# Kernel tuning notes

Measured on AMD Instinct MI355X. Metric: run time of the kernel, lower is better.

The kernel has to match this reference:

```python
import jax, jax.numpy as jnp
import numpy as np

DIM = 512
HEADS = 8
B, H, W = 8, 32, 32
SMOOTH = 1e-4
BN_EPS = 1e-5


def _conv(x, w, pad):
    return jax.lax.conv_general_dilated(
        x, w, window_strides=(1, 1), padding=[(pad, pad), (pad, pad)],
        dimension_numbers=('NCHW', 'OIHW', 'NCHW'))


def setup_inputs() -> dict:
    key = jax.random.key(0)
    k1, k2, k3 = jax.random.split(key, 3)
    x = jax.random.normal(k1, (B, DIM, H, W), dtype=jnp.float32)
    # conv weights with fan-in style scaling for stable magnitudes
    W_qkv = jax.random.normal(k2, (3 * DIM, DIM, 3, 3), dtype=jnp.float32) * (1.0 / np.sqrt(DIM * 9))
    W_out = jax.random.normal(k3, (DIM, DIM, 1, 1), dtype=jnp.float32) * (1.0 / np.sqrt(DIM))
    gamma = jnp.ones((DIM,), dtype=jnp.float32)
    beta = jnp.zeros((DIM,), dtype=jnp.float32)
    return {"x": x, "W_qkv": W_qkv, "W_out": W_out, "gamma": gamma, "beta": beta}


def reference(x, W_qkv, W_out, gamma, beta):
    b, c, h, w = x.shape
    g = HEADS
    d = c // g
    n = h * w
    qkv = _conv(x, W_qkv, pad=1)                      # [b, 3c, h, w]
    q, k, v = jnp.split(qkv, 3, axis=1)
    # 'b (g d) h w -> b g (h w) d'
    to_seq = lambda t: t.reshape(b, g, d, n).transpose(0, 1, 3, 2)
    q, k, v = to_seq(q), to_seq(k), to_seq(v)         # [b, g, n, d]
    attn = jnp.einsum('bgid,bgjd->bgij', q, k)        # [b, g, n, n]
    qn = jnp.sqrt(jnp.sum(q * q, axis=-1) + SMOOTH)   # [b, g, n]
    kn = jnp.sqrt(jnp.sum(k * k, axis=-1) + SMOOTH)   # [b, g, n]
    attn = attn / (qn[:, :, :, None] * kn[:, :, None, :] + SMOOTH)
    out = jnp.einsum('bgij,bgjd->bgid', attn, v)      # [b, g, n, d]
    # 'b g (h w) d -> b (g d) h w'
    out = out.transpose(0, 1, 3, 2).reshape(b, c, h, w)
    out = _conv(out, W_out, pad=0)
    # BatchNorm2d (training mode: batch statistics, biased variance)
    mean = jnp.mean(out, axis=(0, 2, 3))
    var = jnp.var(out, axis=(0, 2, 3))
    out = (out - mean[None, :, None, None]) * jax.lax.rsqrt(var + BN_EPS)[None, :, None, None]
    out = out * gamma[None, :, None, None] + beta[None, :, None, None]
    return jax.nn.relu(out)
```

## Files before the change

kernel.cpp:

```cpp
#include <hip/hip_runtime.h>
#include <math.h>


#define SMOOTH 1e-4f
#define BN_EPS 1e-5f

typedef __attribute__((ext_vector_type(8))) short bf16x8;
typedef __attribute__((ext_vector_type(8))) unsigned short u16x8;
typedef __attribute__((ext_vector_type(4))) float f32x4;
typedef __attribute__((ext_vector_type(4))) unsigned int u32x4;
typedef __attribute__((ext_vector_type(4))) unsigned short u16x4;

__device__ inline unsigned short bf16rne(float f) {
  unsigned int u = __float_as_uint(f);
  u += 0x7fff + ((u >> 16) & 1);
  return (unsigned short)(u >> 16);
}
__device__ inline float b2f(unsigned short u) {
  return __uint_as_float((unsigned int)u << 16);
}

typedef __attribute__((address_space(1))) void gvoid;
typedef __attribute__((address_space(3))) void lvoid;
__device__ __forceinline__ void async16(const void* g, void* l) {
  __builtin_amdgcn_global_load_lds((gvoid*)g, (lvoid*)l, 16, 0, 0);
}

__global__ void prep_kernel(const float* __restrict__ wq,
                            unsigned short* __restrict__ wqr2,
                            const float* __restrict__ x,
                            unsigned short* __restrict__ xrp2,
                            const float* __restrict__ wo,
                            unsigned short* __restrict__ wor,
                            float* __restrict__ sums,
                            float* __restrict__ sumsq) {
  __shared__ float Sh[64 * 132];
  const int tid = threadIdx.x;
  const int bid = blockIdx.x;
  if (bid < 3072) {
    const size_t pair0 = (size_t)bid * 256;
    for (int off = tid; off < 576; off += 256)
      *(float4*)(Sh + off * 4) = *(const float4*)(wq + pair0 * 9 + off * 4);
    __syncthreads();
    const int co = (int)(pair0 >> 9);
    const int ciBase = (int)(pair0 & 511);
    const int cotile = co >> 6, co_l = co & 63;
    for (int idx = tid; idx < 288; idx += 256) {
      int t = idx >> 5;
      int oct = idx & 31;
      int ci = ciBase + oct * 8;
      int ci0c = ci >> 5, c4 = oct & 3;
      u16x8 pk;
#pragma unroll
      for (int e = 0; e < 8; ++e) pk[e] = bf16rne(Sh[(oct * 8 + e) * 9 + t]);
      size_t o = (size_t)(ci0c * 24 + cotile) * 18432 +
                 (size_t)((c4 * 9 + t) * 64 + co_l) * 8;
      *(u16x8*)(wqr2 + o) = pk;
    }
  } else if (bid < 3584) {
    const int bx = bid - 3072;
    const int p0 = (bx & 7) * 128;
    const int ci0 = ((bx >> 3) & 7) * 64;
    const int b = bx >> 6;
    for (int k = 0; k < 8; ++k) {
      int idx = tid + k * 256;
      int c4 = idx & 31, row = idx >> 5;
      *(float4*)(Sh + row * 132 + c4 * 4) =
          *(const float4*)(x + ((size_t)(b * 512 + ci0 + row)) * 1024 + p0 + c4 * 4);
    }
    __syncthreads();
    const int pl = tid >> 1, half = tid & 1;
    const int p = p0 + pl;
    const int h = p >> 5, w = p & 31;
#pragma unroll
    for (int v = 0; v < 8; ++v) {
      u16x4 pk;
#pragma unroll
      for (int e = 0; e < 4; ++e)
        pk[e] = bf16rne(Sh[(half * 32 + v * 4 + e) * 132 + pl]);
      int cc = ci0 + half * 32 + v * 4;
      int ci0c = cc >> 5, c4 = (cc >> 3) & 3, e0 = cc & 7;
      size_t gran =
          (size_t)((ci0c * 4 + c4) * 8 + b) * 1156 + (h + 1) * 34 + (w + 1);
      *(u16x4*)(xrp2 + gran * 8 + e0) = pk;
    }
  } else {
    const int rb = bid - 3584;
    int idx = rb * 256 + tid;
    wor[idx] = bf16rne(wo[idx]);
    if (rb < 2) {
      sums[idx] = 0.f;
      sumsq[idx] = 0.f;
    }
  }
}

__global__ __launch_bounds__(256) void conv3x3_mfma(
    const unsigned short* __restrict__ wqr2,
    const unsigned short* __restrict__ xrp2,
    unsigned short* __restrict__ qt, unsigned short* __restrict__ kt,
    unsigned short* __restrict__ vt, float* __restrict__ rqn,
    float* __restrict__ rkn) {
  __shared__ __align__(16) unsigned short Wl[2304 * 8];
  __shared__ __align__(16) unsigned short Xl[4 * 256 * 8];
  __shared__ float Snl[128];

  const int tid = threadIdx.x;
  const int lane = tid & 63;
  const int wave = tid >> 6;
  const int wco = (wave & 1) * 32;
  const int wn = (wave >> 1) * 64;
  const int l15 = lane & 15;
  const int quad = lane >> 4;
  const int h0 = blockIdx.x * 4;
  const int co0 = blockIdx.y * 64;
  const int b = blockIdx.z;

  f32x4 acc[2][4];
  for (int ma = 0; ma < 2; ++ma)
    for (int nb = 0; nb < 4; ++nb) acc[ma][nb] = (f32x4){0.f, 0.f, 0.f, 0.f};

  for (int ci0 = 0; ci0 < 512; ci0 += 32) {
    const int ci0c = ci0 >> 5;
    __syncthreads();
    const unsigned short* wsrc =
        wqr2 + (size_t)(ci0c * 24 + (co0 >> 6)) * 18432;
    {
      int cbase = wave * 9;
#pragma unroll
      for (int j = 0; j < 9; ++j) {
        int c = cbase + j;
        async16(wsrc + (size_t)c * 512 + lane * 8, Wl + (size_t)c * 512);
      }
    }
    const unsigned short* xsrc =
        xrp2 + ((size_t)((ci0c * 4 + wave) * 8 + b) * 1156 + h0 * 34) * 8;
#pragma unroll
    for (int j = 0; j < 4; ++j)
      async16(xsrc + (size_t)j * 512 + lane * 8,
              Xl + (size_t)(wave * 256 + j * 64) * 8);
    __syncthreads();

#pragma unroll
    for (int t = 0; t < 9; ++t) {
      const int ky = t / 3, kx = t - ky * 3;
      bf16x8 af[2], bfr[4];
#pragma unroll
      for (int ma = 0; ma < 2; ++ma)
        af[ma] = *(const bf16x8*)(
            Wl + (size_t)((quad * 9 + t) * 64 + wco + ma * 16 + l15) * 8);
#pragma unroll
      for (int nb = 0; nb < 4; ++nb) {
        int n = wn + nb * 16 + l15;
        int hh = (n >> 5) + ky;
        int wi = (n & 31) + kx;
        bfr[nb] = *(const bf16x8*)(Xl + (size_t)(quad * 256 + hh * 34 + wi) * 8);
      }
#pragma unroll
      for (int ma = 0; ma < 2; ++ma)
#pragma unroll
        for (int nb = 0; nb < 4; ++nb)
          acc[ma][nb] = __builtin_amdgcn_mfma_f32_16x16x32_bf16(
              af[ma], bfr[nb], acc[ma][nb], 0, 0, 0);
    }
  }

  const int sec = co0 >> 9;
  const int g = (co0 & 511) >> 6;
  const int bg = b * 8 + g;
  if (sec < 2) {
    unsigned short* dst = (sec == 0) ? qt : kt;
#pragma unroll
    for (int ma = 0; ma < 2; ++ma)
#pragma unroll
      for (int nb = 0; nb < 4; ++nb) {
        int n = wn + nb * 16 + l15;
        int p = (h0 + (n >> 5)) * 32 + (n & 31);
        int db = wco + ma * 16 + quad * 4;
        u16x4 pk;
#pragma unroll
        for (int r = 0; r < 4; ++r) pk[r] = bf16rne(acc[ma][nb][r]);
        *(u16x4*)(dst + ((size_t)bg * 1024 + p) * 64 + db) = pk;
      }
    float ps[4];
#pragma unroll
    for (int nb = 0; nb < 4; ++nb) {
      float s = 0.f;
#pragma unroll
      for (int ma = 0; ma < 2; ++ma)
#pragma unroll
        for (int r = 0; r < 4; ++r) s = fmaf(acc[ma][nb][r], acc[ma][nb][r], s);
      s += __shfl_down(s, 32);
      s += __shfl_down(s, 16);
      ps[nb] = s;
    }
    if (wco == 0 && quad == 0)
#pragma unroll
      for (int nb = 0; nb < 4; ++nb) Snl[wn + nb * 16 + l15] = ps[nb];
    __syncthreads();
    if (wco == 32 && quad == 0) {
      float* ndst = (sec == 0) ? rqn : rkn;
#pragma unroll
      for (int nb = 0; nb < 4; ++nb) {
        int n = wn + nb * 16 + l15;
        int p = (h0 + (n >> 5)) * 32 + (n & 31);
        ndst[bg * 1024 + p] = rsqrtf(Snl[n] + ps[nb] + SMOOTH);
      }
    }
  } else {
#pragma unroll
    for (int ma = 0; ma < 2; ++ma)
#pragma unroll
      for (int nb = 0; nb < 4; ++nb) {
        int n = wn + nb * 16 + l15;
        int p = (h0 + (n >> 5)) * 32 + (n & 31);
#pragma unroll
        for (int r = 0; r < 4; ++r) {
          int d = wco + ma * 16 + quad * 4 + r;
          vt[((size_t)bg * 64 + d) * 1024 + p] = bf16rne(acc[ma][nb][r]);
        }
      }
  }
}

__global__ __launch_bounds__(256) void attn_mfma(
    const unsigned short* __restrict__ qt, const unsigned short* __restrict__ kt,
    const unsigned short* __restrict__ vt, const float* __restrict__ rqn,
    const float* __restrict__ rkn, unsigned short* __restrict__ aob) {
  __shared__ __align__(16) unsigned short Kl[64 * 72];
  __shared__ __align__(16) unsigned short Vl[64 * 72];
  __shared__ __align__(16) unsigned short Sl[64 * 72];

  const int tid = threadIdx.x;
  const int lane = tid & 63, wave = tid >> 6;
  const int l15 = lane & 15, quad = lane >> 4;
  const int bg = blockIdx.x;
  const int i0 = blockIdx.y * 64;
  const int iw = i0 + wave * 16;
  const int b = bg >> 3, g = bg & 7;

  bf16x8 qf[2];
#pragma unroll
  for (int ks = 0; ks < 2; ++ks)
    qf[ks] = *(const bf16x8*)(
        qt + ((size_t)bg * 1024 + iw + l15) * 64 + ks * 32 + quad * 8);

  float rq[4];
#pragma unroll
  for (int r = 0; r < 4; ++r) rq[r] = rqn[bg * 1024 + iw + quad * 4 + r];

  f32x4 oacc[4];
  for (int nf = 0; nf < 4; ++nf) oacc[nf] = (f32x4){0.f, 0.f, 0.f, 0.f};

  unsigned short* Sw = Sl + wave * 16 * 72;

  for (int jt = 0; jt < 16; ++jt) {
    const int j0 = jt * 64;
    __syncthreads();
    for (int idx = tid; idx < 512; idx += 256) {
      int c8 = idx & 7, row = idx >> 3;
      *(u32x4*)(Kl + row * 72 + c8 * 8) =
          *(const u32x4*)(kt + ((size_t)bg * 1024 + j0 + row) * 64 + c8 * 8);
      *(u32x4*)(Vl + row * 72 + c8 * 8) =
          *(const u32x4*)(vt + ((size_t)bg * 64 + row) * 1024 + j0 + c8 * 8);
    }
    __syncthreads();

    f32x4 sacc[4];
    for (int nb = 0; nb < 4; ++nb) sacc[nb] = (f32x4){0.f, 0.f, 0.f, 0.f};
#pragma unroll
    for (int ks = 0; ks < 2; ++ks) {
#pragma unroll
      for (int nb = 0; nb < 4; ++nb) {
        bf16x8 kf = *(const bf16x8*)(Kl + (l15 + 16 * nb) * 72 + ks * 32 + quad * 8);
        sacc[nb] = __builtin_amdgcn_mfma_f32_16x16x32_bf16(
            qf[ks], kf, sacc[nb], 0, 0, 0);
      }
    }

#pragma unroll
    for (int nb = 0; nb < 4; ++nb) {
      float rk = rkn[bg * 1024 + j0 + l15 + 16 * nb];
#pragma unroll
      for (int r = 0; r < 4; ++r) {
        float s = sacc[nb][r] * (rq[r] * rk);
        Sw[(quad * 4 + r) * 72 + l15 + 16 * nb] = bf16rne(s);
      }
    }
#pragma unroll
    for (int ks2 = 0; ks2 < 2; ++ks2) {
      bf16x8 sa = *(const bf16x8*)(Sw + l15 * 72 + ks2 * 32 + quad * 8);
#pragma unroll
      for (int nf = 0; nf < 4; ++nf) {
        bf16x8 vb = *(const bf16x8*)(Vl + (l15 + 16 * nf) * 72 + ks2 * 32 + quad * 8);
        oacc[nf] = __builtin_amdgcn_mfma_f32_16x16x32_bf16(sa, vb, oacc[nf], 0, 0, 0);
      }
    }
  }

#pragma unroll
  for (int nf = 0; nf < 4; ++nf)
#pragma unroll
    for (int r = 0; r < 4; ++r) {
      int i = iw + quad * 4 + r;
      int d = l15 + 16 * nf;
      aob[((size_t)(b * 1024) + i) * 512 + g * 64 + d] = bf16rne(oacc[nf][r]);
    }
}

__global__ __launch_bounds__(256) void conv1x1_mfma(
    const unsigned short* __restrict__ wor, const unsigned short* __restrict__ aob,
    unsigned short* __restrict__ yb, float* __restrict__ sums,
    float* __restrict__ sumsq) {
  __shared__ __align__(16) unsigned short Wl[64 * 40];
  __shared__ __align__(16) unsigned short Bl[64 * 40];

  const int tid = threadIdx.x;
  const int lane = tid & 63, wave = tid >> 6;
  const int l15 = lane & 15, quad = lane >> 4;
  const int wco = (wave & 1) * 32;
  const int wp = (wave >> 1) * 32;
  const int p0 = blockIdx.x * 64;
  const int co0 = blockIdx.y * 64;
  const int b = blockIdx.z;

  f32x4 acc[2][2];
  for (int ma = 0; ma < 2; ++ma)
    for (int nb = 0; nb < 2; ++nb) acc[ma][nb] = (f32x4){0.f, 0.f, 0.f, 0.f};

  for (int ci0 = 0; ci0 < 512; ci0 += 32) {
    __syncthreads();
    {
      int c4 = tid & 3, co = tid >> 2;
      *(u32x4*)(Wl + co * 40 + c4 * 8) =
          *(const u32x4*)(wor + (size_t)(co0 + co) * 512 + ci0 + c4 * 8);
      *(u32x4*)(Bl + co * 40 + c4 * 8) =
          *(const u32x4*)(aob + ((size_t)(b * 1024) + p0 + co) * 512 + ci0 + c4 * 8);
    }
    __syncthreads();

    bf16x8 af[2], bf[2];
#pragma unroll
    for (int ma = 0; ma < 2; ++ma)
      af[ma] = *(const bf16x8*)(Wl + (wco + ma * 16 + l15) * 40 + quad * 8);
#pragma unroll
    for (int nb = 0; nb < 2; ++nb)
      bf[nb] = *(const bf16x8*)(Bl + (wp + nb * 16 + l15) * 40 + quad * 8);
#pragma unroll
    for (int ma = 0; ma < 2; ++ma)
#pragma unroll
      for (int nb = 0; nb < 2; ++nb)
        acc[ma][nb] = __builtin_amdgcn_mfma_f32_16x16x32_bf16(
            af[ma], bf[nb], acc[ma][nb], 0, 0, 0);
  }

#pragma unroll
  for (int ma = 0; ma < 2; ++ma)
#pragma unroll
    for (int r = 0; r < 4; ++r) {
      int co = co0 + wco + ma * 16 + quad * 4 + r;
      float s1 = 0.f, s2 = 0.f;
#pragma unroll
      for (int nb = 0; nb < 2; ++nb) {
        float v = acc[ma][nb][r];
        yb[((size_t)(b * 512) + co) * 1024 + p0 + wp + nb * 16 + l15] = bf16rne(v);
        s1 += v;
        s2 = fmaf(v, v, s2);
      }
      for (int off = 8; off >= 1; off >>= 1) {
        s1 += __shfl_down(s1, off, 16);
        s2 += __shfl_down(s2, off, 16);
      }
      if (l15 == 0) {
        atomicAdd(&sums[co], s1);
        atomicAdd(&sumsq[co], s2);
      }
    }
}

__global__ void bn_kernel(const unsigned short* __restrict__ yb,
                          const float* __restrict__ sums,
                          const float* __restrict__ sumsq,
                          const float* __restrict__ gamma,
                          const float* __restrict__ beta,
                          float* __restrict__ out) {
  int idx = blockIdx.x * 256 + threadIdx.x;
  int c = (idx >> 8) & 511;
  u16x4 vb = *(const u16x4*)(yb + (size_t)idx * 4);
  float mean = sums[c] * (1.f / 8192.f);
  float var = sumsq[c] * (1.f / 8192.f) - mean * mean;
  float sc = gamma[c] * rsqrtf(var + BN_EPS);
  float sh = beta[c] - mean * sc;
  float4 r;
  r.x = fmaxf(0.f, fmaf(b2f(vb[0]), sc, sh));
  r.y = fmaxf(0.f, fmaf(b2f(vb[1]), sc, sh));
  r.z = fmaxf(0.f, fmaf(b2f(vb[2]), sc, sh));
  r.w = fmaxf(0.f, fmaf(b2f(vb[3]), sc, sh));
  ((float4*)out)[idx] = r;
}

extern "C" void kernel_launch(void* const* d_in, const int* in_sizes, int n_in,
                              void* d_out, int out_size, void* d_ws,
                              size_t ws_size, hipStream_t stream) {
  const float* x = (const float*)d_in[0];
  const float* wq = (const float*)d_in[1];
  const float* wo = (const float*)d_in[2];
  const float* gamma = (const float*)d_in[3];
  const float* beta = (const float*)d_in[4];
  float* out = (float*)d_out;

  unsigned short* qt = (unsigned short*)d_ws;
  unsigned short* kt = qt + (size_t)4194304;
  unsigned short* vt = kt + (size_t)4194304;
  unsigned short* aob = vt + (size_t)4194304;
  unsigned short* wqr2 = aob + (size_t)4194304;
  unsigned short* wor = wqr2 + (size_t)7077888;
  unsigned short* xrp2 = wor + (size_t)262144;
  float* rqn = (float*)(xrp2 + (size_t)4736000);
  float* rkn = rqn + 65536;
  unsigned short* yb = (unsigned short*)(rkn + 65536);
  float* sums = (float*)(yb + (size_t)4194304);
  float* sumsq = sums + 512;

  hipMemsetAsync(xrp2, 0, (size_t)4736000 * 2, stream);
  prep_kernel<<<dim3(4608), 256, 0, stream>>>(wq, wqr2, x, xrp2, wo, wor, sums,
                                              sumsq);
  conv3x3_mfma<<<dim3(8, 24, 8), 256, 0, stream>>>(wqr2, xrp2, qt, kt, vt, rqn,
                                                   rkn);
  attn_mfma<<<dim3(64, 16), 256, 0, stream>>>(qt, kt, vt, rqn, rkn, aob);
  conv1x1_mfma<<<dim3(16, 8, 8), 256, 0, stream>>>(wor, aob, yb, sums, sumsq);
  bn_kernel<<<dim3(4096), 256, 0, stream>>>(yb, sums, sumsq, gamma, beta, out);
}
```

Before: 294.4 us.

## Prefetch next K/V tile into registers and vectorize score stores via row permutation

The attention kernel now loads the next K/V tile from global memory into registers while the current tile is being computed, so global latency overlaps with the MFMA work. K rows are stored to shared memory in a permuted order, which lets each lane own 4 consecutive key columns. The scaled scores can then be packed into one 8-byte shared store per row, with a single float4 load of the key norms. This costs extra registers per thread, which may lower occupancy.

```diff
diff --git a/kernel.cpp b/kernel.cpp
--- a/kernel.cpp
+++ b/kernel.cpp
@@ -239,6 +239,11 @@
   const int iw = i0 + wave * 16;
   const int b = bg >> 3, g = bg & 7;
 
+  const int c8a = tid & 7, rowa = tid >> 3;
+  const int c8b = c8a, rowb = rowa + 32;
+  const int pra = (rowa & 3) * 16 + (rowa >> 2);
+  const int prb = (rowb & 3) * 16 + (rowb >> 2);
+
   bf16x8 qf[2];
 #pragma unroll
   for (int ks = 0; ks < 2; ++ks)
@@ -254,15 +259,26 @@
 
   unsigned short* Sw = Sl + wave * 16 * 72;
 
+  u32x4 rk0, rk1, rv0, rv1;
+  rk0 = *(const u32x4*)(kt + ((size_t)bg * 1024 + 0 + rowa) * 64 + c8a * 8);
+  rk1 = *(const u32x4*)(kt + ((size_t)bg * 1024 + 0 + rowb) * 64 + c8b * 8);
+  rv0 = *(const u32x4*)(vt + ((size_t)bg * 64 + rowa) * 1024 + 0 + c8a * 8);
+  rv1 = *(const u32x4*)(vt + ((size_t)bg * 64 + rowb) * 1024 + 0 + c8b * 8);
+
   for (int jt = 0; jt < 16; ++jt) {
     const int j0 = jt * 64;
     __syncthreads();
-    for (int idx = tid; idx < 512; idx += 256) {
-      int c8 = idx & 7, row = idx >> 3;
-      *(u32x4*)(Kl + row * 72 + c8 * 8) =
-          *(const u32x4*)(kt + ((size_t)bg * 1024 + j0 + row) * 64 + c8 * 8);
-      *(u32x4*)(Vl + row * 72 + c8 * 8) =
-          *(const u32x4*)(vt + ((size_t)bg * 64 + row) * 1024 + j0 + c8 * 8);
+    *(u32x4*)(Kl + pra * 72 + c8a * 8) = rk0;
+    *(u32x4*)(Kl + prb * 72 + c8b * 8) = rk1;
+    *(u32x4*)(Vl + rowa * 72 + c8a * 8) = rv0;
+    *(u32x4*)(Vl + rowb * 72 + c8b * 8) = rv1;
+    u32x4 nk0, nk1, nv0, nv1;
+    if (jt < 15) {
+      const int j1 = j0 + 64;
+      nk0 = *(const u32x4*)(kt + ((size_t)bg * 1024 + j1 + rowa) * 64 + c8a * 8);
+      nk1 = *(const u32x4*)(kt + ((size_t)bg * 1024 + j1 + rowb) * 64 + c8b * 8);
+      nv0 = *(const u32x4*)(vt + ((size_t)bg * 64 + rowa) * 1024 + j1 + c8a * 8);
+      nv1 = *(const u32x4*)(vt + ((size_t)bg * 64 + rowb) * 1024 + j1 + c8b * 8);
     }
     __syncthreads();
 
@@ -272,20 +288,21 @@
     for (int ks = 0; ks < 2; ++ks) {
 #pragma unroll
       for (int nb = 0; nb < 4; ++nb) {
-        bf16x8 kf = *(const bf16x8*)(Kl + (l15 + 16 * nb) * 72 + ks * 32 + quad * 8);
+        bf16x8 kf = *(const bf16x8*)(Kl + (nb * 16 + l15) * 72 + ks * 32 + quad * 8);
         sacc[nb] = __builtin_amdgcn_mfma_f32_16x16x32_bf16(
             qf[ks], kf, sacc[nb], 0, 0, 0);
       }
     }
 
-#pragma unroll
-    for (int nb = 0; nb < 4; ++nb) {
-      float rk = rkn[bg * 1024 + j0 + l15 + 16 * nb];
-#pragma unroll
-      for (int r = 0; r < 4; ++r) {
-        float s = sacc[nb][r] * (rq[r] * rk);
-        Sw[(quad * 4 + r) * 72 + l15 + 16 * nb] = bf16rne(s);
-      }
+    float4 rk4 = *(const float4*)(rkn + bg * 1024 + j0 + 4 * l15);
+#pragma unroll
+    for (int r = 0; r < 4; ++r) {
+      u16x4 pk;
+      pk[0] = bf16rne(sacc[0][r] * (rq[r] * rk4.x));
+      pk[1] = bf16rne(sacc[1][r] * (rq[r] * rk4.y));
+      pk[2] = bf16rne(sacc[2][r] * (rq[r] * rk4.z));
+      pk[3] = bf16rne(sacc[3][r] * (rq[r] * rk4.w));
+      *(u16x4*)(Sw + (quad * 4 + r) * 72 + 4 * l15) = pk;
     }
 #pragma unroll
     for (int ks2 = 0; ks2 < 2; ++ks2) {
@@ -295,6 +312,9 @@
         bf16x8 vb = *(const bf16x8*)(Vl + (l15 + 16 * nf) * 72 + ks2 * 32 + quad * 8);
         oacc[nf] = __builtin_amdgcn_mfma_f32_16x16x32_bf16(sa, vb, oacc[nf], 0, 0, 0);
       }
+    }
+    if (jt < 15) {
+      rk0 = nk0; rk1 = nk1; rv0 = nv0; rv1 = nv1;
     }
   }
 
```

After: 291.5 us. No clear change (-1.0%).

## Double-buffer K/V in registers, 2x M per wave in attention, retile weight prep

Applied to the files above, without the earlier changes.

The attention kernel now runs 128 threads per block, with each wave computing 32 query rows. This lets each K/V fragment loaded from LDS feed two MFMAs. The next K/V tile is prefetched into registers while the current tile is being computed, and K rows are permuted so the scaled scores can be written as packed 4-wide stores with a single float4 load of rkn. The weight-reorder part of prep_kernel is retiled: each block handles a 32-output-channel by 32-input-channel slab with coalesced loads, so the grid shrinks. The costs are higher register pressure and fewer waves per block, which may lower occupancy.

```diff
diff --git a/kernel.cpp b/kernel.cpp
--- a/kernel.cpp
+++ b/kernel.cpp
@@ -34,31 +34,41 @@
                             unsigned short* __restrict__ wor,
                             float* __restrict__ sums,
                             float* __restrict__ sumsq) {
-  __shared__ float Sh[64 * 132];
+  __shared__ float Sh[32 * 292];
   const int tid = threadIdx.x;
   const int bid = blockIdx.x;
-  if (bid < 3072) {
-    const size_t pair0 = (size_t)bid * 256;
-    for (int off = tid; off < 576; off += 256)
-      *(float4*)(Sh + off * 4) = *(const float4*)(wq + pair0 * 9 + off * 4);
-    __syncthreads();
-    const int co = (int)(pair0 >> 9);
-    const int ciBase = (int)(pair0 & 511);
-    const int cotile = co >> 6, co_l = co & 63;
-    for (int idx = tid; idx < 288; idx += 256) {
-      int t = idx >> 5;
-      int oct = idx & 31;
-      int ci = ciBase + oct * 8;
-      int ci0c = ci >> 5, c4 = oct & 3;
-      u16x8 pk;
-#pragma unroll
-      for (int e = 0; e < 8; ++e) pk[e] = bf16rne(Sh[(oct * 8 + e) * 9 + t]);
-      size_t o = (size_t)(ci0c * 24 + cotile) * 18432 +
-                 (size_t)((c4 * 9 + t) * 64 + co_l) * 8;
-      *(u16x8*)(wqr2 + o) = pk;
-    }
-  } else if (bid < 3584) {
-    const int bx = bid - 3072;
+  if (bid < 768) {
+    const int cotile = bid / 32;
+    const int rem = bid - cotile * 32;
+    const int ci0c = rem >> 1, cohalf = rem & 1;
+#pragma unroll
+    for (int k = 0; k < 9; ++k) {
+      int idx = tid + k * 256;
+      int row = idx / 72, col = idx - row * 72;
+      *(float4*)(Sh + row * 292 + col * 4) =
+          *(const float4*)(wq +
+                           (size_t)(cotile * 64 + cohalf * 32 + row) * 4608 +
+                           ci0c * 288 + col * 4);
+    }
+    __syncthreads();
+    const size_t wbase = (size_t)(ci0c * 24 + cotile) * 18432;
+#pragma unroll
+    for (int k = 0; k < 5; ++k) {
+      int j = tid + k * 256;
+      if (j < 1152) {
+        int co_l = j & 31;
+        int g36 = j >> 5;
+        int c4 = g36 / 9, tt = g36 - c4 * 9;
+        u16x8 pk;
+#pragma unroll
+        for (int e = 0; e < 8; ++e)
+          pk[e] = bf16rne(Sh[co_l * 292 + (c4 * 8 + e) * 9 + tt]);
+        *(u16x8*)(wqr2 + wbase +
+                  (size_t)((c4 * 9 + tt) * 64 + cohalf * 32 + co_l) * 8) = pk;
+      }
+    }
+  } else if (bid < 1280) {
+    const int bx = bid - 768;
     const int p0 = (bx & 7) * 128;
     const int ci0 = ((bx >> 3) & 7) * 64;
     const int b = bx >> 6;
@@ -85,7 +95,7 @@
       *(u16x4*)(xrp2 + gran * 8 + e0) = pk;
     }
   } else {
-    const int rb = bid - 3584;
+    const int rb = bid - 1280;
     int idx = rb * 256 + tid;
     wor[idx] = bf16rne(wo[idx]);
     if (rb < 2) {
@@ -223,7 +233,7 @@
   }
 }
 
-__global__ __launch_bounds__(256) void attn_mfma(
+__global__ __launch_bounds__(128) void attn_mfma(
     const unsigned short* __restrict__ qt, const unsigned short* __restrict__ kt,
     const unsigned short* __restrict__ vt, const float* __restrict__ rqn,
     const float* __restrict__ rkn, unsigned short* __restrict__ aob) {
@@ -236,76 +246,126 @@
   const int l15 = lane & 15, quad = lane >> 4;
   const int bg = blockIdx.x;
   const int i0 = blockIdx.y * 64;
-  const int iw = i0 + wave * 16;
+  const int iw = i0 + wave * 32;
   const int b = bg >> 3, g = bg & 7;
 
-  bf16x8 qf[2];
-#pragma unroll
-  for (int ks = 0; ks < 2; ++ks)
-    qf[ks] = *(const bf16x8*)(
-        qt + ((size_t)bg * 1024 + iw + l15) * 64 + ks * 32 + quad * 8);
-
-  float rq[4];
-#pragma unroll
-  for (int r = 0; r < 4; ++r) rq[r] = rqn[bg * 1024 + iw + quad * 4 + r];
-
-  f32x4 oacc[4];
-  for (int nf = 0; nf < 4; ++nf) oacc[nf] = (f32x4){0.f, 0.f, 0.f, 0.f};
-
-  unsigned short* Sw = Sl + wave * 16 * 72;
+  int srow[4], sperm[4], sc8[4];
+#pragma unroll
+  for (int s = 0; s < 4; ++s) {
+    int gidx = tid + s * 128;
+    sc8[s] = gidx & 7;
+    srow[s] = gidx >> 3;
+    sperm[s] = (srow[s] & 3) * 16 + (srow[s] >> 2);
+  }
+
+  bf16x8 qf[2][2];
+#pragma unroll
+  for (int ma = 0; ma < 2; ++ma)
+#pragma unroll
+    for (int ks = 0; ks < 2; ++ks)
+      qf[ma][ks] = *(const bf16x8*)(
+          qt + ((size_t)bg * 1024 + iw + ma * 16 + l15) * 64 + ks * 32 + quad * 8);
+
+  float rq[2][4];
+#pragma unroll
+  for (int ma = 0; ma < 2; ++ma)
+#pragma unroll
+    for (int r = 0; r < 4; ++r)
+      rq[ma][r] = rqn[bg * 1024 + iw + ma * 16 + quad * 4 + r];
+
+  f32x4 oacc[2][4];
+  for (int mf = 0; mf < 2; ++mf)
+    for (int nf = 0; nf < 4; ++nf) oacc[mf][nf] = (f32x4){0.f, 0.f, 0.f, 0.f};
+
+  unsigned short* Sw = Sl + wave * 32 * 72;
+
+  u32x4 rk[4], rv[4];
+#pragma unroll
+  for (int s = 0; s < 4; ++s) {
+    rk[s] = *(const u32x4*)(kt + ((size_t)bg * 1024 + srow[s]) * 64 + sc8[s] * 8);
+    rv[s] = *(const u32x4*)(vt + ((size_t)bg * 64 + srow[s]) * 1024 + sc8[s] * 8);
+  }
 
   for (int jt = 0; jt < 16; ++jt) {
     const int j0 = jt * 64;
     __syncthreads();
-    for (int idx = tid; idx < 512; idx += 256) {
-      int c8 = idx & 7, row = idx >> 3;
-      *(u32x4*)(Kl + row * 72 + c8 * 8) =
-          *(const u32x4*)(kt + ((size_t)bg * 1024 + j0 + row) * 64 + c8 * 8);
-      *(u32x4*)(Vl + row * 72 + c8 * 8) =
-          *(const u32x4*)(vt + ((size_t)bg * 64 + row) * 1024 + j0 + c8 * 8);
-    }
-    __syncthreads();
-
-    f32x4 sacc[4];
-    for (int nb = 0; nb < 4; ++nb) sacc[nb] = (f32x4){0.f, 0.f, 0.f, 0.f};
+#pragma unroll
+    for (int s = 0; s < 4; ++s) {
+      *(u32x4*)(Kl + sperm[s] * 72 + sc8[s] * 8) = rk[s];
+      *(u32x4*)(Vl + srow[s] * 72 + sc8[s] * 8) = rv[s];
+    }
+    u32x4 nk[4], nv[4];
+    if (jt < 15) {
+      const int j1 = j0 + 64;
+#pragma unroll
+      for (int s = 0; s < 4; ++s) {
+        nk[s] = *(const u32x4*)(kt + ((size_t)bg * 1024 + j1 + srow[s]) * 64 + sc8[s] * 8);
+        nv[s] = *(const u32x4*)(vt + ((size_t)bg * 64 + srow[s]) * 1024 + j1 + sc8[s] * 8);
+      }
+    }
+    __syncthreads();
+
+    f32x4 sacc[2][4];
+    for (int ma = 0; ma < 2; ++ma)
+      for (int nb = 0; nb < 4; ++nb) sacc[ma][nb] = (f32x4){0.f, 0.f, 0.f, 0.f};
 #pragma unroll
     for (int ks = 0; ks < 2; ++ks) {
 #pragma unroll
       for (int nb = 0; nb < 4; ++nb) {
-        bf16x8 kf = *(const bf16x8*)(Kl + (l15 + 16 * nb) * 72 + ks * 32 + quad * 8);
-        sacc[nb] = __builtin_amdgcn_mfma_f32_16x16x32_bf16(
-            qf[ks], kf, sacc[nb], 0, 0, 0);
-      }
-    }
-
-#pragma unroll
-    for (int nb = 0; nb < 4; ++nb) {
-      float rk = rkn[bg * 1024 + j0 + l15 + 16 * nb];
+        bf16x8 kf = *(const bf16x8*)(Kl + (nb * 16 + l15) * 72 + ks * 32 + quad * 8);
+#pragma unroll
+        for (int ma = 0; ma < 2; ++ma)
+          sacc[ma][nb] = __builtin_amdgcn_mfma_f32_16x16x32_bf16(
+              qf[ma][ks], kf, sacc[ma][nb], 0, 0, 0);
+      }
+    }
+
+    float4 rk4 = *(const float4*)(rkn + bg * 1024 + j0 + 4 * l15);
+#pragma unroll
+    for (int ma = 0; ma < 2; ++ma)
 #pragma unroll
       for (int r = 0; r < 4; ++r) {
-        float s = sacc[nb][r] * (rq[r] * rk);
-        Sw[(quad * 4 + r) * 72 + l15 + 16 * nb] = bf16rne(s);
-      }
-    }
+        u16x4 pk;
+        pk[0] = bf16rne(sacc[ma][0][r] * (rq[ma][r] * rk4.x));
+        pk[1] = bf16rne(sacc[ma][1][r] * (rq[ma][r] * rk4.y));
+        pk[2] = bf16rne(sacc[ma][2][r] * (rq[ma][r] * rk4.z));
+        pk[3] = bf16rne(sacc[ma][3][r] * (rq[ma][r] * rk4.w));
+        *(u16x4*)(Sw + (ma * 16 + quad * 4 + r) * 72 + 4 * l15) = pk;
+      }
 #pragma unroll
     for (int ks2 = 0; ks2 < 2; ++ks2) {
-      bf16x8 sa = *(const bf16x8*)(Sw + l15 * 72 + ks2 * 32 + quad * 8);
+      bf16x8 sa[2];
+#pragma unroll
+      for (int mf = 0; mf < 2; ++mf)
+        sa[mf] = *(const bf16x8*)(Sw + (mf * 16 + l15) * 72 + ks2 * 32 + quad * 8);
 #pragma unroll
       for (int nf = 0; nf < 4; ++nf) {
         bf16x8 vb = *(const bf16x8*)(Vl + (l15 + 16 * nf) * 72 + ks2 * 32 + quad * 8);
-        oacc[nf] = __builtin_amdgcn_mfma_f32_16x16x32_bf16(sa, vb, oacc[nf], 0, 0, 0);
-      }
-    }
-  }
-
-#pragma unroll
-  for (int nf = 0; nf < 4; ++nf)
-#pragma unroll
-    for (int r = 0; r < 4; ++r) {
-      int i = iw + quad * 4 + r;
-      int d = l15 + 16 * nf;
-      aob[((size_t)(b * 1024) + i) * 512 + g * 64 + d] = bf16rne(oacc[nf][r]);
-    }
+#pragma unroll
+        for (int mf = 0; mf < 2; ++mf)
+          oacc[mf][nf] = __builtin_amdgcn_mfma_f32_16x16x32_bf16(
+              sa[mf], vb, oacc[mf][nf], 0, 0, 0);
+      }
+    }
+    if (jt < 15) {
+#pragma unroll
+      for (int s = 0; s < 4; ++s) {
+        rk[s] = nk[s];
+        rv[s] = nv[s];
+      }
+    }
+  }
+
+#pragma unroll
+  for (int mf = 0; mf < 2; ++mf)
+#pragma unroll
+    for (int nf = 0; nf < 4; ++nf)
+#pragma unroll
+      for (int r = 0; r < 4; ++r) {
+        int i = iw + mf * 16 + quad * 4 + r;
+        int d = l15 + 16 * nf;
+        aob[((size_t)(b * 1024) + i) * 512 + g * 64 + d] = bf16rne(oacc[mf][nf][r]);
+      }
 }
 
 __global__ __launch_bounds__(256) void conv1x1_mfma(
@@ -423,11 +483,11 @@
   float* sumsq = sums + 512;
 
   hipMemsetAsync(xrp2, 0, (size_t)4736000 * 2, stream);
-  prep_kernel<<<dim3(4608), 256, 0, stream>>>(wq, wqr2, x, xrp2, wo, wor, sums,
+  prep_kernel<<<dim3(2304), 256, 0, stream>>>(wq, wqr2, x, xrp2, wo, wor, sums,
                                               sumsq);
   conv3x3_mfma<<<dim3(8, 24, 8), 256, 0, stream>>>(wqr2, xrp2, qt, kt, vt, rqn,
                                                    rkn);
-  attn_mfma<<<dim3(64, 16), 256, 0, stream>>>(qt, kt, vt, rqn, rkn, aob);
+  attn_mfma<<<dim3(64, 16), 128, 0, stream>>>(qt, kt, vt, rqn, rkn, aob);
   conv1x1_mfma<<<dim3(16, 8, 8), 256, 0, stream>>>(wor, aob, yb, sums, sumsq);
   bn_kernel<<<dim3(4096), 256, 0, stream>>>(yb, sums, sumsq, gamma, beta, out);
 }
```

New measurement: 271.6 us (median of 2 runs). 7.7% less time.
